# Kernel tuning notes

Hardware: AMD Instinct MI355X
Metric: run time of the kernel (lower is better)

The kernel has to match this reference:

```python
import jax, jax.numpy as jnp
import numpy as np

N = 32768          # total proposals (batch of images concatenated)
C = 81             # num classes (class 0 = background)
K = 4096           # fixed candidate budget for masked NMS (jit-friendly)
SCORE_THRESH = 0.05
NMS_THRESH = 0.5
IMG_W, IMG_H = 1333.0, 800.0   # image size for clip_to_image
CLS_OFFSET = 4096.0            # > max coord: offsets boxes per label so NMS is per-class


def setup_inputs() -> dict:
    key = jax.random.key(0)
    k1, k2, k3 = jax.random.split(key, 3)
    x = jax.random.normal(k1, (N, C), dtype=jnp.float32)
    xy = jax.random.uniform(k2, (N, 2), dtype=jnp.float32) * jnp.array([IMG_W * 0.9, IMG_H * 0.9], jnp.float32)
    wh = 4.0 + jax.random.uniform(k3, (N, 2), dtype=jnp.float32) * 124.0
    boxes = jnp.concatenate([xy, xy + wh], axis=-1)  # [N,4] xyxy
    return {"x": x, "boxes": boxes}


def _pairwise_iou(b):
    # b: [K,4] xyxy -> [K,K] IoU
    x1, y1, x2, y2 = b[:, 0], b[:, 1], b[:, 2], b[:, 3]
    area = (x2 - x1) * (y2 - y1)
    iw = jnp.maximum(jnp.minimum(x2[:, None], x2[None, :]) - jnp.maximum(x1[:, None], x1[None, :]), 0.0)
    ih = jnp.maximum(jnp.minimum(y2[:, None], y2[None, :]) - jnp.maximum(y1[:, None], y1[None, :]), 0.0)
    inter = iw * ih
    return inter / (area[:, None] + area[None, :] - inter + 1e-9)


def reference(x, boxes):
    # softmax scores
    prob = jax.nn.softmax(x, axis=-1)                    # [N,C]
    # clip_to_image (remove_empty=False)
    bx = jnp.stack([
        jnp.clip(boxes[:, 0], 0.0, IMG_W - 1),
        jnp.clip(boxes[:, 1], 0.0, IMG_H - 1),
        jnp.clip(boxes[:, 2], 0.0, IMG_W - 1),
        jnp.clip(boxes[:, 3], 0.0, IMG_H - 1)], axis=-1)  # [N,4]
    # score threshold + drop background (label 0), as in filter_results
    valid = (prob > SCORE_THRESH) & (jnp.arange(C)[None, :] != 0)
    flat = jnp.where(valid, prob, -1.0).reshape(-1)       # [N*C]
    vals, idx = jax.lax.top_k(flat, K)                    # sorted desc
    box_idx = idx // C
    labels = idx % C                                      # [K] int
    bk = bx[box_idx]                                      # [K,4] (boxes repeated per class in torch code)
    keep0 = vals > 0.0                                    # invalid slots padded with -1
    # multi-label NMS: offset boxes by label so different classes never overlap
    boff = bk + (labels.astype(bk.dtype) * CLS_OFFSET)[:, None]
    iou_gt = _pairwise_iou(boff) > NMS_THRESH             # [K,K] bool
    order = jnp.arange(K)

    def step(keep, i):
        sup = keep[i] & (order > i) & iou_gt[i]
        return keep & ~sup, None

    keep, _ = jax.lax.scan(step, keep0, order)
    dets = jnp.where(keep[:, None],
                     jnp.concatenate([bk, vals[:, None]], axis=-1),
                     0.0)                                 # [K,5] = xyxy + score
    return dets, labels, keep
```

## Files before the change

### kernel.cpp

```cpp
#include <hip/hip_runtime.h>

#pragma clang fp contract(off)

typedef unsigned int u32;
typedef unsigned long long u64;
typedef long long i64;

#define N_ROWS 32768
#define NCLS 81
#define TOPK 4096
#define IMGW_M1 1332.0f
#define IMGH_M1 799.0f

#define CAND_THREADS 256
#define RPB 32
#define CAND_GRID (N_ROWS / RPB)
#define CPT 11
#define BLK_CAND_CAP 640
#define ROW_F4 ((RPB * NCLS) / 4)

#define H1_BASE 0x3D4Cu
#define H1_BINS 576

#define NSLICE 32
#define SUBCAP 384
#define SEG_LDS 4096

#define MCAP 1024
#define MMAX 512
#define NW32 16

__device__ inline double fast_exp_neg(double d) {
    if (d < -45.0) return 0.0;
    const double L2E    = 1.4426950408889634074;
    const double LN2_HI = 6.93147180369123816490e-01;
    const double LN2_LO = 1.90821492927058770002e-10;
    double n = __builtin_rint(d * L2E);
    double r = __builtin_fma(-n, LN2_HI, d);
    r = __builtin_fma(-n, LN2_LO, r);
    double p = 1.0 / 6227020800.0;
    p = __builtin_fma(p, r, 1.0 / 479001600.0);
    p = __builtin_fma(p, r, 1.0 / 39916800.0);
    p = __builtin_fma(p, r, 1.0 / 3628800.0);
    p = __builtin_fma(p, r, 1.0 / 362880.0);
    p = __builtin_fma(p, r, 1.0 / 40320.0);
    p = __builtin_fma(p, r, 1.0 / 5040.0);
    p = __builtin_fma(p, r, 1.0 / 720.0);
    p = __builtin_fma(p, r, 1.0 / 120.0);
    p = __builtin_fma(p, r, 1.0 / 24.0);
    p = __builtin_fma(p, r, 1.0 / 6.0);
    p = __builtin_fma(p, r, 0.5);
    p = __builtin_fma(p, r, 1.0);
    p = __builtin_fma(p, r, 1.0);
    i64 ni = (i64)n;
    double sc = __longlong_as_double((i64)(1023 + ni) << 52);
    return p * sc;
}

__global__ void __launch_bounds__(256) k_cand(const float* __restrict__ x,
                                              u32* __restrict__ binCur,
                                              u64* __restrict__ selBins) {
    __shared__ float4 lx4[ROW_F4];
    __shared__ u32 lK[BLK_CAND_CAP];
    __shared__ u32 lI[BLK_CAND_CAP];
    __shared__ u32 lcnt;
    float* lx = (float*)lx4;
    const int t = threadIdx.x;
    if (t == 0) lcnt = 0;

    const float4* xv = (const float4*)x + (size_t)blockIdx.x * ROW_F4;
    for (int i = t; i < ROW_F4; i += CAND_THREADS) lx4[i] = xv[i];
    __syncthreads();

    const int rl = t >> 3;
    const int q = t & 7;
    const int c0 = q * 10;
    const int cEff = (q == 7) ? 11 : 10;
    const int row = blockIdx.x * RPB + rl;
    const float* xr = lx + rl * NCLS;

    float v[CPT];
    #pragma unroll
    for (int i = 0; i < CPT; i++) v[i] = (i < cEff) ? xr[c0 + i] : -1.0e30f;

    float m = v[0];
    #pragma unroll
    for (int i = 1; i < CPT; i++) m = fmaxf(m, v[i]);
    m = fmaxf(m, __shfl_xor(m, 1));
    m = fmaxf(m, __shfl_xor(m, 2));
    m = fmaxf(m, __shfl_xor(m, 4));

    double e[CPT];
    #pragma unroll
    for (int i = 0; i < CPT; i++) {
        if (i < cEff) {
            float d = v[i] - m;
            e[i] = fast_exp_neg((double)d);
        } else e[i] = 0.0;
    }
    double s = 0.0;
    #pragma unroll
    for (int i = 0; i < CPT; i++) if (i < cEff) s += e[i];
    s += __shfl_xor(s, 1);
    s += __shfl_xor(s, 2);
    s += __shfl_xor(s, 4);

    const double THRMID = (double)0.05f + 0x1.0p-29;
    double ethr = THRMID * s;
    #pragma unroll
    for (int i = 0; i < CPT; i++) {
        int c = c0 + i;
        if (i < cEff && c != 0 && e[i] > ethr) {
            float pf = (float)(e[i] / s);
            u32 slot = atomicAdd(&lcnt, 1u);
            lK[slot] = __float_as_uint(pf);
            lI[slot] = (u32)(row * NCLS + c);
        }
    }
    __syncthreads();

    const u32 tot = lcnt;
    const u32 sbase = (blockIdx.x & (NSLICE - 1)) * H1_BINS;
    for (u32 i = t; i < tot; i += CAND_THREADS) {
        u32 key = lK[i];
        u32 b = (key >> 16) - H1_BASE;
        u32 pos = atomicAdd(&binCur[sbase + b], 1u);
        if (pos < (u32)SUBCAP)
            selBins[(size_t)(sbase + b) * SUBCAP + pos] =
                ((u64)key << 32) | (u64)(0xFFFFFFFFu - lI[i]);
    }
}

__global__ void __launch_bounds__(1024) k_midlite(const u32* __restrict__ binCur,
                                                  u32* __restrict__ sufG) {
    __shared__ u32 cs[1024];
    int t = threadIdx.x;
    u32 s1 = 0;
    if (t < H1_BINS) {
        for (int j = 0; j < NSLICE; j++) s1 += binCur[j * H1_BINS + t];
    }
    cs[t] = (t < H1_BINS) ? s1 : 0u;
    __syncthreads();
    for (int d = 1; d < 1024; d <<= 1) {
        u32 v = (t + d < 1024) ? cs[t + d] : 0u;
        __syncthreads();
        cs[t] += v;
        __syncthreads();
    }
    if (t < 577) sufG[t] = cs[t];
    u32 S_t = cs[t];
    u32 S_next = (t < 1023) ? cs[t + 1] : 0u;
    if (S_next < TOPK && S_t >= TOPK) sufG[577] = (u32)t;
}

__global__ void __launch_bounds__(256) k_binrank(const u64* __restrict__ selBins,
                                                 const u32* __restrict__ binCur,
                                                 const u32* __restrict__ sufG,
                                                 const float* __restrict__ boxes,
                                                 float* __restrict__ rboxes,
                                                 float* __restrict__ rvals,
                                                 int* __restrict__ rlabel,
                                                 float* __restrict__ out) {
    __shared__ u64 seg[SEG_LDS];
    __shared__ u32 sBase[NSLICE + 1];
    const int t = threadIdx.x;
    const u32 B = sufG[577];

    if (blockIdx.x == H1_BINS) {
        u32 covered = sufG[B];
        if (covered > (u32)TOPK) covered = TOPK;
        for (u32 r = covered + t; r < TOPK; r += 256) {
            rboxes[r * 4 + 0] = 0; rboxes[r * 4 + 1] = 0;
            rboxes[r * 4 + 2] = 0; rboxes[r * 4 + 3] = 0;
            rvals[r] = 0.0f; rlabel[r] = 0;
            out[TOPK * 5 + r] = 0.0f;
            out[TOPK * 6 + r] = 0.0f;
            float* d = out + (size_t)r * 5;
            d[0] = 0; d[1] = 0; d[2] = 0; d[3] = 0; d[4] = 0;
        }
        return;
    }

    const u32 b = blockIdx.x;
    if (b < B) return;
    u32 start = sufG[b + 1];
    u32 end = sufG[b];
    if (start >= end) return;
    if (start >= (u32)TOPK) return;

    if (t < NSLICE) {
        u32 c0s = binCur[t * H1_BINS + b];
        if (c0s > (u32)SUBCAP) c0s = SUBCAP;
        u32 inc = c0s;
        #pragma unroll
        for (int d = 1; d < NSLICE; d <<= 1) {
            u32 o = __shfl_up(inc, d);
            if (t >= d) inc += o;
        }
        sBase[t] = inc - c0s;
        if (t == NSLICE - 1) sBase[NSLICE] = inc;
    }
    __syncthreads();
    const u32 lenSt = sBase[NSLICE];
    const u32 ldsLen = lenSt < (u32)SEG_LDS ? lenSt : (u32)SEG_LDS;
    {
        const u32 s = (u32)t >> 3;
        const u32 base = sBase[s];
        const u32 cntS = sBase[s + 1] - base;
        const u64* gs = selBins + ((size_t)s * H1_BINS + b) * SUBCAP;
        for (u32 i = (u32)t & 7u; i < cntS; i += 8u) {
            u32 d = base + i;
            if (d < (u32)SEG_LDS) seg[d] = gs[i];
        }
    }
    __syncthreads();

    for (u32 i = (u32)t; i < ldsLen; i += 256) {
        u64 c = seg[i];
        u32 r0 = 0;
        for (u32 j = 0; j < ldsLen; j++) r0 += (seg[j] > c) ? 1u : 0u;
        u32 r = start + r0;
        if (r >= (u32)TOPK) continue;
        u32 idx = 0xFFFFFFFFu - (u32)(c & 0xFFFFFFFFull);
        float val = __uint_as_float((u32)(c >> 32));
        u32 bi = idx / NCLS;
        u32 lab = idx % NCLS;
        const float* bp = boxes + (size_t)bi * 4;
        float x1 = fminf(fmaxf(bp[0], 0.0f), IMGW_M1);
        float y1 = fminf(fmaxf(bp[1], 0.0f), IMGH_M1);
        float x2 = fminf(fmaxf(bp[2], 0.0f), IMGW_M1);
        float y2 = fminf(fmaxf(bp[3], 0.0f), IMGH_M1);
        rboxes[r * 4 + 0] = x1; rboxes[r * 4 + 1] = y1;
        rboxes[r * 4 + 2] = x2; rboxes[r * 4 + 3] = y2;
        rvals[r] = val;
        rlabel[r] = (int)lab;
        out[TOPK * 5 + r] = (float)lab;
    }
}

__device__ inline float4 nms_box(u32 g, const float4* __restrict__ boxL,
                                 const float* __restrict__ rboxes,
                                 const unsigned short* __restrict__ memRank, float off) {
    if (g < (u32)MCAP) return boxL[g];
    float4 b = ((const float4*)rboxes)[memRank[g]];
    return make_float4(b.x + off, b.y + off, b.z + off, b.w + off);
}
__device__ inline float nms_area(u32 g, const float* __restrict__ areaL, float4 b) {
    if (g < (u32)MCAP) return areaL[g];
    return (b.z - b.x) * (b.w - b.y);
}

__global__ void __launch_bounds__(256) k_nms(const float* __restrict__ rboxes,
                                             const float* __restrict__ rvals,
                                             const int* __restrict__ rlabel,
                                             float* __restrict__ out) {
    int c = blockIdx.x + 1;
    __shared__ int lLab[TOPK];
    __shared__ float4 boxL[MCAP];
    __shared__ float areaL[MCAP];
    __shared__ unsigned short memRank[TOPK];
    __shared__ u32 colW[MMAX * NW32];
    __shared__ u32 remOut[NW32];
    __shared__ unsigned char keepL[TOPK];
    __shared__ u32 cc[64];
    __shared__ u32 baseC[64];
    __shared__ u32 mTotSh;
    const int t = threadIdx.x;
    const int w = t >> 6, lane = t & 63;
    const u64 laneLT = ((u64)1 << lane) - 1;
    const float off = (float)c * 4096.0f;

    {
        const int4* g4 = (const int4*)rlabel;
        int4* l4 = (int4*)lLab;
        for (int i = t; i < TOPK / 4; i += 256) l4[i] = g4[i];
    }
    __syncthreads();

    for (int it = 0; it < 16; it++) {
        int chunk = it * 4 + w;
        int r = chunk * 64 + lane;
        u64 mask = __ballot(lLab[r] == c);
        if (lane == 0) cc[chunk] = (u32)__popcll(mask);
    }
    __syncthreads();
    if (t < 64) {
        u32 v = cc[t];
        u32 inc = v;
        #pragma unroll
        for (int d = 1; d < 64; d <<= 1) {
            u32 o = __shfl_up(inc, d);
            if (lane >= d) inc += o;
        }
        baseC[t] = inc - v;
        if (t == 63) mTotSh = inc;
    }
    __syncthreads();
    const u32 m = mTotSh;
    for (int it = 0; it < 16; it++) {
        int chunk = it * 4 + w;
        int r = chunk * 64 + lane;
        bool match = (lLab[r] == c);
        u64 mask = __ballot(match);
        if (match) {
            u32 g = baseC[chunk] + (u32)__popcll(mask & laneLT);
            memRank[g] = (unsigned short)r;
            if (g < (u32)MCAP) {
                float4 b = ((const float4*)rboxes)[r];
                float bx1 = b.x + off, by1 = b.y + off;
                float bx2 = b.z + off, by2 = b.w + off;
                boxL[g] = make_float4(bx1, by1, bx2, by2);
                areaL[g] = (bx2 - bx1) * (by2 - by1);
            }
        }
    }
    __syncthreads();

    const bool matrixPath = (m <= (u32)MMAX);
    if (matrixPath) {
        const u32 nW = (m + 31) >> 5;
        const u32 items = m * nW;
        for (u32 p = t; p < items; p += 256) {
            u32 s = p / nW;
            u32 wd = p - s * nW;
            float4 bs = nms_box(s, boxL, rboxes, memRank, off);
            float as = nms_area(s, areaL, bs);
            u32 word = 0;
            u32 j0 = wd << 5;
            u32 jend = j0 + 32; if (jend > m) jend = m;
            u32 js = (j0 > s + 1) ? j0 : (s + 1);
            for (u32 j = js; j < jend; j++) {
                float4 bj = nms_box(j, boxL, rboxes, memRank, off);
                float aj = nms_area(j, areaL, bj);
                float iw = fmaxf(fminf(bs.z, bj.z) - fmaxf(bs.x, bj.x), 0.0f);
                float ih = fmaxf(fminf(bs.w, bj.w) - fmaxf(bs.y, bj.y), 0.0f);
                float inter = iw * ih;
                float iou = inter / (as + aj - inter + 1e-9f);
                if (iou > 0.5f) word |= (1u << (j - j0));
            }
            colW[s * NW32 + wd] = word;
        }
        __syncthreads();
        if (t < 64) {
            u32 remW = 0;
            bool own = ((u32)lane < ((m + 31) >> 5));
            for (u32 s2 = 0; s2 < m; s2++) {
                u32 rw = __shfl(remW, (int)(s2 >> 5));
                bool removed = (rw >> (s2 & 31)) & 1u;
                u32 cw = own ? colW[s2 * NW32 + lane] : 0u;
                if (!removed) remW |= cw;
            }
            if (own) remOut[lane] = remW;
        }
        __syncthreads();
    } else {
        for (u32 q2 = t; q2 < m; q2 += 256) keepL[q2] = 1;
        __syncthreads();
        for (u32 i = 0; i < m; i++) {
            __syncthreads();
            if (!keepL[i]) continue;
            float4 bi = nms_box(i, boxL, rboxes, memRank, off);
            float ai = nms_area(i, areaL, bi);
            for (u32 jj = i + 1 + t; jj < m; jj += 256) {
                if (!keepL[jj]) continue;
                float4 bj = nms_box(jj, boxL, rboxes, memRank, off);
                float aj = nms_area(jj, areaL, bj);
                float iw = fmaxf(fminf(bi.z, bj.z) - fmaxf(bi.x, bj.x), 0.0f);
                float ih = fmaxf(fminf(bi.w, bj.w) - fmaxf(bi.y, bj.y), 0.0f);
                float inter = iw * ih;
                float iou = inter / (ai + aj - inter + 1e-9f);
                if (iou > 0.5f) keepL[jj] = 0;
            }
        }
        __syncthreads();
    }

    for (u32 q2 = t; q2 < m; q2 += 256) {
        bool keep = matrixPath ? !((remOut[q2 >> 5] >> (q2 & 31)) & 1u)
                               : (keepL[q2] != 0);
        int r = memRank[q2];
        out[TOPK * 6 + r] = keep ? 1.0f : 0.0f;
        float* d = out + (size_t)r * 5;
        if (keep) {
            float4 b = ((const float4*)rboxes)[r];
            d[0] = b.x; d[1] = b.y; d[2] = b.z; d[3] = b.w;
            d[4] = rvals[r];
        } else {
            d[0] = 0; d[1] = 0; d[2] = 0; d[3] = 0; d[4] = 0;
        }
    }
}

extern "C" void kernel_launch(void* const* d_in, const int* in_sizes, int n_in,
                              void* d_out, int out_size, void* d_ws, size_t ws_size,
                              hipStream_t stream) {
    const float* x = (const float*)d_in[0];
    const float* boxes = (const float*)d_in[1];
    float* out = (float*)d_out;

    u32* W = (u32*)d_ws;
    u32* sufG = W + 16;
    u32* binCur = W + 1024;
    u64* selBins = (u64*)((char*)d_ws + 131072);
    float* rboxes = (float*)(selBins + (size_t)NSLICE * H1_BINS * SUBCAP);
    float* rvals = rboxes + 4 * TOPK;
    int* rlabel = (int*)(rvals + TOPK);

    hipMemsetAsync(W, 0, 4096 + NSLICE * H1_BINS * sizeof(u32), stream);
    k_cand<<<CAND_GRID, CAND_THREADS, 0, stream>>>(x, binCur, selBins);
    k_midlite<<<1, 1024, 0, stream>>>(binCur, sufG);
    k_binrank<<<H1_BINS + 1, 256, 0, stream>>>(selBins, binCur, sufG, boxes,
                                               rboxes, rvals, rlabel, out);
    k_nms<<<80, 256, 0, stream>>>(rboxes, rvals, rlabel, out);
}
```

Baseline: 94.91 us.

## Sub-bucket bin entries by secondary key byte to shrink O(n^2) rank loop

Inside each histogram bin, candidates are first counted into a 256-bucket sub-histogram keyed on the next 8 bits of the score, suffix-scanned, and scattered into LDS grouped by sub-bucket. Each element's rank then only compares against entries in its own sub-bucket plus the count of all higher buckets, instead of against the whole bin. This cuts the quadratic comparison work, at the cost of an extra global read pass, LDS atomics and a 256-step scan with many barriers. If the buffer is truncated at SEG_LDS, the sub-bucket offsets may no longer match what was actually stored.

```diff
diff --git a/kernel.cpp b/kernel.cpp
--- a/kernel.cpp
+++ b/kernel.cpp
@@ -162,6 +162,8 @@
                                                  int* __restrict__ rlabel,
                                                  float* __restrict__ out) {
     __shared__ u64 seg[SEG_LDS];
+    __shared__ u32 h2[256];
+    __shared__ u32 cur2[256];
     __shared__ u32 sBase[NSLICE + 1];
     const int t = threadIdx.x;
     const u32 B = sufG[577];
@@ -200,25 +202,51 @@
         sBase[t] = inc - c0s;
         if (t == NSLICE - 1) sBase[NSLICE] = inc;
     }
+    h2[t] = 0;
+    cur2[t] = 0;
     __syncthreads();
     const u32 lenSt = sBase[NSLICE];
     const u32 ldsLen = lenSt < (u32)SEG_LDS ? lenSt : (u32)SEG_LDS;
+
     {
         const u32 s = (u32)t >> 3;
-        const u32 base = sBase[s];
-        const u32 cntS = sBase[s + 1] - base;
+        const u32 cntS = sBase[s + 1] - sBase[s];
         const u64* gs = selBins + ((size_t)s * H1_BINS + b) * SUBCAP;
         for (u32 i = (u32)t & 7u; i < cntS; i += 8u) {
-            u32 d = base + i;
-            if (d < (u32)SEG_LDS) seg[d] = gs[i];
+            u32 s2 = (u32)(gs[i] >> 40) & 0xFFu;
+            atomicAdd(&h2[s2], 1u);
+        }
+    }
+    __syncthreads();
+    for (int d = 1; d < 256; d <<= 1) {
+        u32 o = (t + d < 256) ? h2[t + d] : 0u;
+        __syncthreads();
+        h2[t] += o;
+        __syncthreads();
+    }
+
+    {
+        const u32 s = (u32)t >> 3;
+        const u32 cntS = sBase[s + 1] - sBase[s];
+        const u64* gs = selBins + ((size_t)s * H1_BINS + b) * SUBCAP;
+        for (u32 i = (u32)t & 7u; i < cntS; i += 8u) {
+            u64 c = gs[i];
+            u32 s2 = (u32)(c >> 40) & 0xFFu;
+            u32 lo = (s2 < 255u) ? h2[s2 + 1] : 0u;
+            u32 pos = lo + atomicAdd(&cur2[s2], 1u);
+            if (pos < (u32)SEG_LDS) seg[pos] = c;
         }
     }
     __syncthreads();
 
     for (u32 i = (u32)t; i < ldsLen; i += 256) {
         u64 c = seg[i];
-        u32 r0 = 0;
-        for (u32 j = 0; j < ldsLen; j++) r0 += (seg[j] > c) ? 1u : 0u;
+        u32 s2 = (u32)(c >> 40) & 0xFFu;
+        u32 lo = (s2 < 255u) ? h2[s2 + 1] : 0u;
+        u32 hi = h2[s2];
+        if (hi > ldsLen) hi = ldsLen;
+        u32 r0 = lo;
+        for (u32 j = lo; j < hi; j++) r0 += (seg[j] > c) ? 1u : 0u;
         u32 r = start + r0;
         if (r >= (u32)TOPK) continue;
         u32 idx = 0xFFFFFFFFu - (u32)(c & 0xFFFFFFFFull);
```

Result: no change. 94.38 us (-0.6%).
